# Performance work log

Measured on AMD Instinct MI355X. Metric: run time of the kernel, lower is better.

Reference implementation:

```python
import jax, jax.numpy as jnp
import numpy as np

V, H, F, E, S, N, O = 50000, 1024, 4096, 8, 128, 4096, 2


def setup_inputs() -> dict:
    key = jax.random.key(0)
    ks = jax.random.split(key, 9)
    x = jax.random.randint(ks[0], (N, S), 0, V)
    emb = jax.random.normal(ks[1], (V, H), dtype=jnp.float32) * 0.02
    emb = emb.at[0].set(0.0)  # padding_idx=0
    Wg = jax.random.normal(ks[2], (H, E), dtype=jnp.float32) * 0.02
    W1 = jax.random.normal(ks[3], (E, H, F), dtype=jnp.float32) * 0.02
    b1 = jnp.zeros((E, F), dtype=jnp.float32)
    W2 = jax.random.normal(ks[4], (E, F, H), dtype=jnp.float32) * 0.02
    b2 = jnp.zeros((E, H), dtype=jnp.float32)
    Wfc = jax.random.normal(ks[5], (H, O), dtype=jnp.float32) * 0.02
    bfc = jnp.zeros((O,), dtype=jnp.float32)
    return {"x": x, "emb": emb, "Wg": Wg, "W1": W1, "b1": b1,
            "W2": W2, "b2": b2, "Wfc": Wfc, "bfc": bfc}


def reference(x, emb, Wg, W1, b1, W2, b2, Wfc, bfc):
    # embedding lookup + mean pool over sequence: [N, S, H] -> [N, H]
    h = emb[x].mean(axis=1)
    # top-1 gating (deepspeed MoE default k=1)
    gates = jax.nn.softmax(h @ Wg, axis=-1)              # [N, E]
    idx = jnp.argmax(gates, axis=-1)                      # [N]
    onehot = jax.nn.one_hot(idx, E, dtype=h.dtype)        # [N, E]
    combine = gates * onehot                              # [N, E] top-1 prob
    # dense-dispatch reference for grouped expert GEMMs (FFN: H->F->H, ReLU)
    h1 = jax.nn.relu(jnp.einsum('nh,ehf->nef', h, W1) + b1)  # [N, E, F]
    h2 = jnp.einsum('nef,efh->neh', h1, W2) + b2             # [N, E, H]
    moe = jnp.einsum('ne,neh->nh', combine, h2)              # [N, H]
    return jax.nn.log_softmax(moe @ Wfc + bfc, axis=1)       # [N, O]
```

## Files before the change

kernel.cpp:

```cpp
#include <hip/hip_runtime.h>
#include <stdint.h>

#define V_SZ 50000
#define H_DIM 1024
#define F_DIM 4096
#define E_NUM 8
#define S_LEN 128
#define N_TOK 4096
#define NPAD (N_TOK + E_NUM*128)
#define EMB_SCALE 16.0f
#define SK2 4

typedef unsigned short u16;
typedef unsigned int u32;
typedef unsigned char u8;
typedef short bf16x8 __attribute__((ext_vector_type(8)));
typedef float f32x4 __attribute__((ext_vector_type(4)));
typedef float f32x2 __attribute__((ext_vector_type(2)));

__device__ __forceinline__ u16 f2bf(float f) {
  u32 u = __builtin_bit_cast(u32, f);
  u += 0x7fffu + ((u >> 16) & 1u);
  return (u16)(u >> 16);
}
__device__ __forceinline__ u32 pack2(float a, float b) {
  return (u32)f2bf(a) | ((u32)f2bf(b) << 16);
}

__device__ __forceinline__ void gld_lds16(u16* lds, const u16* g) {
  __builtin_amdgcn_global_load_lds((const __attribute__((address_space(1))) void*)g,
                                   (__attribute__((address_space(3))) void*)lds,
                                   16, 0, 0);
}

__global__ void embconv_kernel(const float* __restrict__ emb, u8* __restrict__ embf8) {
  const size_t total = (size_t)V_SZ*H_DIM/8;
  const size_t stride = (size_t)gridDim.x*blockDim.x;
  for (size_t i = (size_t)blockIdx.x*blockDim.x + threadIdx.x; i < total; i += stride) {
    const float4 a = ((const float4*)emb)[i*2];
    const float4 b = ((const float4*)emb)[i*2+1];
    u32 w0, w1;
    w0 = __builtin_amdgcn_cvt_pk_fp8_f32(a.x*EMB_SCALE, a.y*EMB_SCALE, 0u, false);
    w0 = __builtin_amdgcn_cvt_pk_fp8_f32(a.z*EMB_SCALE, a.w*EMB_SCALE, w0, true);
    w1 = __builtin_amdgcn_cvt_pk_fp8_f32(b.x*EMB_SCALE, b.y*EMB_SCALE, 0u, false);
    w1 = __builtin_amdgcn_cvt_pk_fp8_f32(b.z*EMB_SCALE, b.w*EMB_SCALE, w1, true);
    ((uint2*)embf8)[i] = make_uint2(w0, w1);
  }
}

__global__ void poolgate_kernel(const int* __restrict__ x, const u8* __restrict__ embf8,
                                const float* __restrict__ Wg,
                                u16* __restrict__ hB, float* __restrict__ gate_val,
                                int* __restrict__ gate_idx, int* __restrict__ cnt) {
  __shared__ int sidx[S_LEN];
  __shared__ float wsum[4][8];
  const int n = blockIdx.x, t = threadIdx.x;
  if (t < S_LEN) sidx[t] = x[n*S_LEN + t];
  __syncthreads();
  float a0 = 0.f, a1 = 0.f, a2 = 0.f, a3 = 0.f;
  #pragma unroll 8
  for (int s = 0; s < S_LEN; ++s) {
    const u32 w = *(const u32*)(embf8 + (size_t)sidx[s]*H_DIM + t*4);
    const f32x2 lo = __builtin_amdgcn_cvt_pk_f32_fp8(w, false);
    const f32x2 hi = __builtin_amdgcn_cvt_pk_f32_fp8(w, true);
    a0 += lo[0]; a1 += lo[1]; a2 += hi[0]; a3 += hi[1];
  }
  const float sc = 1.0f/((float)S_LEN * EMB_SCALE);
  a0 *= sc; a1 *= sc; a2 *= sc; a3 *= sc;
  uint2 pk; pk.x = pack2(a0, a1); pk.y = pack2(a2, a3);
  *(uint2*)&hB[(size_t)n*H_DIM + t*4] = pk;
  float lg[E_NUM];
  #pragma unroll
  for (int e = 0; e < E_NUM; ++e) lg[e] = 0.f;
  const float hv[4] = {a0, a1, a2, a3};
  #pragma unroll
  for (int j = 0; j < 4; ++j) {
    const float4* w4 = (const float4*)(Wg + (size_t)(t*4+j)*E_NUM);
    const float4 wa = w4[0], wb = w4[1];
    lg[0] += hv[j]*wa.x; lg[1] += hv[j]*wa.y; lg[2] += hv[j]*wa.z; lg[3] += hv[j]*wa.w;
    lg[4] += hv[j]*wb.x; lg[5] += hv[j]*wb.y; lg[6] += hv[j]*wb.z; lg[7] += hv[j]*wb.w;
  }
  #pragma unroll
  for (int m = 32; m >= 1; m >>= 1) {
    #pragma unroll
    for (int e = 0; e < E_NUM; ++e) lg[e] += __shfl_xor(lg[e], m);
  }
  if ((t & 63) == 0) {
    #pragma unroll
    for (int e = 0; e < E_NUM; ++e) wsum[t >> 6][e] = lg[e];
  }
  __syncthreads();
  if (t == 0) {
    float l[E_NUM];
    #pragma unroll
    for (int e = 0; e < E_NUM; ++e)
      l[e] = wsum[0][e] + wsum[1][e] + wsum[2][e] + wsum[3][e];
    float mx = l[0]; int im = 0;
    #pragma unroll
    for (int e = 1; e < E_NUM; ++e) if (l[e] > mx) { mx = l[e]; im = e; }
    float s = 0.f;
    #pragma unroll
    for (int e = 0; e < E_NUM; ++e) s += expf(l[e] - mx);
    gate_val[n] = 1.0f / s;
    gate_idx[n] = im;
    atomicAdd(&cnt[im], 1);
  }
}

__global__ void offsets_kernel(const int* __restrict__ cnt, int* __restrict__ pad_off) {
  int o = 0;
  for (int e = 0; e < E_NUM; ++e) {
    pad_off[e] = o;
    o += ((cnt[e] + 127) >> 7) << 7;
  }
  pad_off[E_NUM] = o;
}

__global__ void scatterconv_kernel(const u16* __restrict__ hB, const int* __restrict__ gate_idx,
                                   const int* __restrict__ pad_off, int* __restrict__ cursor,
                                   int* __restrict__ perm, u16* __restrict__ Hg) {
  __shared__ int srow;
  const int n = blockIdx.x, t = threadIdx.x;
  if (t == 0) {
    const int e = gate_idx[n];
    const int pos = atomicAdd(&cursor[e], 1);
    const int row = pad_off[e] + pos;
    perm[row] = n;
    srow = row;
  }
  __syncthreads();
  const int row = srow;
  const uint4 v = *(const uint4*)(hB + (size_t)n*H_DIM + t*8);
  *(uint4*)&Hg[(size_t)row*H_DIM + t*8] = v;
}

template<int C, int RPER>
__global__ void ct_kernel(const float* __restrict__ in, u16* __restrict__ out) {
  __shared__ float tile[64][65];
  const int c0 = blockIdx.x*64, r0 = blockIdx.y*64;
  const int t = threadIdx.x;
  const int cq = t & 15, rr = t >> 4;
  #pragma unroll
  for (int p = 0; p < 4; ++p) {
    const int row = p*16 + rr;
    float4 v = ((const float4*)(in + (size_t)(r0+row)*C + c0))[cq];
    tile[row][cq*4+0] = v.x; tile[row][cq*4+1] = v.y;
    tile[row][cq*4+2] = v.z; tile[row][cq*4+3] = v.w;
  }
  __syncthreads();
  const int slot = t & 7, nn = t >> 3;
  const int e = r0 / RPER, rl0 = r0 % RPER;
  u16* outE = out + (size_t)e*C*RPER;
  #pragma unroll
  for (int p = 0; p < 2; ++p) {
    const int nc = p*32 + nn;
    uint4 q;
    q.x = pack2(tile[slot*8+0][nc], tile[slot*8+1][nc]);
    q.y = pack2(tile[slot*8+2][nc], tile[slot*8+3][nc]);
    q.z = pack2(tile[slot*8+4][nc], tile[slot*8+5][nc]);
    q.w = pack2(tile[slot*8+6][nc], tile[slot*8+7][nc]);
    *(uint4*)&outE[(size_t)(c0+nc)*RPER + rl0 + slot*8] = q;
  }
}

template<int KTOT, int EPI, int SK>
__launch_bounds__(256, 2)
__global__ void gemm_kernel(const u16* __restrict__ A, const u16* __restrict__ B,
                            const float* __restrict__ bias,
                            const int* __restrict__ perm,
                            const int* __restrict__ pad_off,
                            const int* __restrict__ cnt,
                            u16* __restrict__ out_bf, float* __restrict__ out_f) {
  constexpr int MD = (EPI == 1) ? F_DIM : H_DIM;
  const int e  = blockIdx.z / SK;
  const int kc = blockIdx.z % SK;
  const int seg0 = pad_off[e], seg1 = pad_off[e+1];
  if ((int)blockIdx.y*128 >= seg1 - seg0) return;
  const int t0 = seg0 + blockIdx.y*128;
  const int f0 = blockIdx.x*128;
  const u16* Ae = A + (size_t)e*MD*KTOT;

  __shared__ u16 As[128*64];
  __shared__ u16 Bs[128*64];

  const int tid = threadIdx.x;
  const int lane = tid & 63, wave = tid >> 6;
  const int wm = wave >> 1, wn = wave & 1;

  f32x4 acc[4][4];
  #pragma unroll
  for (int i = 0; i < 4; ++i)
    #pragma unroll
    for (int j = 0; j < 4; ++j) acc[i][j] = (f32x4){0.f, 0.f, 0.f, 0.f};

  const int rsub = lane >> 3, slot = lane & 7;
  const int csw = slot ^ rsub;
  const int fr = lane & 15, fg = lane >> 4;

  const int kbeg = kc*(KTOT/SK), kend = kbeg + KTOT/SK;
  for (int kk = kbeg; kk < kend; kk += 64) {
    __syncthreads();
    #pragma unroll
    for (int i = 0; i < 4; ++i) {
      const int chunk = wave*4 + i;
      const int r = chunk*8 + rsub;
      gld_lds16(&As[chunk*512], Ae + (size_t)(f0 + r)*KTOT + kk + csw*8);
      gld_lds16(&Bs[chunk*512], B  + (size_t)(t0 + r)*KTOT + kk + csw*8);
    }
    __syncthreads();
    #pragma unroll
    for (int kh = 0; kh < 2; ++kh) {
      bf16x8 av[4], bv[4];
      #pragma unroll
      for (int mi = 0; mi < 4; ++mi) {
        const int ra = wm*64 + mi*16 + fr;
        const int sa = (kh*4 + fg) ^ (ra & 7);
        av[mi] = *(const bf16x8*)&As[ra*64 + sa*8];
      }
      #pragma unroll
      for (int ni = 0; ni < 4; ++ni) {
        const int rb = wn*64 + ni*16 + fr;
        const int sb = (kh*4 + fg) ^ (rb & 7);
        bv[ni] = *(const bf16x8*)&Bs[rb*64 + sb*8];
      }
      #pragma unroll
      for (int mi = 0; mi < 4; ++mi)
        #pragma unroll
        for (int ni = 0; ni < 4; ++ni)
          acc[mi][ni] = __builtin_amdgcn_mfma_f32_16x16x32_bf16(av[mi], bv[ni], acc[mi][ni], 0, 0, 0);
    }
  }

  #pragma unroll
  for (int mi = 0; mi < 4; ++mi) {
    const int gm0 = f0 + wm*64 + mi*16 + fg*4;
    #pragma unroll
    for (int ni = 0; ni < 4; ++ni) {
      const int gn = wn*64 + ni*16 + fr;
      if constexpr (EPI == 1) {
        const float* bp = bias + (size_t)e*MD + gm0;
        const float v0 = fmaxf(acc[mi][ni][0] + bp[0], 0.f);
        const float v1 = fmaxf(acc[mi][ni][1] + bp[1], 0.f);
        const float v2 = fmaxf(acc[mi][ni][2] + bp[2], 0.f);
        const float v3 = fmaxf(acc[mi][ni][3] + bp[3], 0.f);
        uint2 pk; pk.x = pack2(v0, v1); pk.y = pack2(v2, v3);
        *(uint2*)&out_bf[(size_t)(t0 + gn)*F_DIM + gm0] = pk;
      } else {
        const int local = blockIdx.y*128 + gn;
        if (local < cnt[e]) {
          const int tok = perm[t0 + gn];
          float* plane = out_f + (size_t)kc*N_TOK*H_DIM;
          *(f32x4*)&plane[(size_t)tok*H_DIM + gm0] = acc[mi][ni];
        }
      }
    }
  }
}

__global__ void final_kernel(const float* __restrict__ planes,
                             const float* __restrict__ b2,
                             const int* __restrict__ gate_idx,
                             const float* __restrict__ gate_val,
                             const float* __restrict__ Wfc,
                             const float* __restrict__ bfc, float* __restrict__ out) {
  const int n = blockIdx.x, l = threadIdx.x;
  const int e = gate_idx[n];
  const float g = gate_val[n];
  const size_t pstride = (size_t)N_TOK*H_DIM/4;
  const float4* p0 = (const float4*)planes + (size_t)n*(H_DIM/4);
  const float4* b24 = (const float4*)(b2 + (size_t)e*H_DIM);
  const float2* w2 = (const float2*)Wfc;
  float a0 = 0.f, a1 = 0.f;
  #pragma unroll
  for (int j = 0; j < H_DIM/256; ++j) {
    const int i4 = j*64 + l;
    const float4 q0 = p0[i4];
    const float4 q1 = p0[i4 + pstride];
    const float4 q2 = p0[i4 + 2*pstride];
    const float4 q3 = p0[i4 + 3*pstride];
    const float4 bb = b24[i4];
    const float vx = (q0.x+q1.x+q2.x+q3.x + bb.x)*g;
    const float vy = (q0.y+q1.y+q2.y+q3.y + bb.y)*g;
    const float vz = (q0.z+q1.z+q2.z+q3.z + bb.z)*g;
    const float vw = (q0.w+q1.w+q2.w+q3.w + bb.w)*g;
    const int hh = i4*4;
    const float2 r0 = w2[hh], r1 = w2[hh+1], r2 = w2[hh+2], r3 = w2[hh+3];
    a0 += vx*r0.x + vy*r1.x + vz*r2.x + vw*r3.x;
    a1 += vx*r0.y + vy*r1.y + vz*r2.y + vw*r3.y;
  }
  #pragma unroll
  for (int m = 32; m >= 1; m >>= 1) { a0 += __shfl_xor(a0, m); a1 += __shfl_xor(a1, m); }
  if (l == 0) {
    const float l0 = a0 + bfc[0], l1 = a1 + bfc[1];
    const float mx = fmaxf(l0, l1);
    const float lse = mx + logf(expf(l0 - mx) + expf(l1 - mx));
    out[(size_t)n*2 + 0] = l0 - lse;
    out[(size_t)n*2 + 1] = l1 - lse;
  }
}

extern "C" void kernel_launch(void* const* d_in, const int* in_sizes, int n_in,
                              void* d_out, int out_size, void* d_ws, size_t ws_size,
                              hipStream_t stream) {
  const int*   x   = (const int*)  d_in[0];
  const float* emb = (const float*)d_in[1];
  const float* Wg  = (const float*)d_in[2];
  const float* W1  = (const float*)d_in[3];
  const float* b1  = (const float*)d_in[4];
  const float* W2  = (const float*)d_in[5];
  const float* b2  = (const float*)d_in[6];
  const float* Wfc = (const float*)d_in[7];
  const float* bfc = (const float*)d_in[8];
  float* out = (float*)d_out;

  char* p = (char*)d_ws;
  size_t off = 0;
  auto alloc = [&](size_t bytes) {
    void* r = p + off;
    off = (off + bytes + 255) & ~(size_t)255;
    return r;
  };
  u16*   hB       = (u16*)  alloc((size_t)N_TOK*H_DIM*2);
  float* gate_val = (float*)alloc((size_t)N_TOK*4);
  int*   gate_idx = (int*)  alloc((size_t)N_TOK*4);
  int*   perm     = (int*)  alloc((size_t)NPAD*4);
  int*   meta     = (int*)  alloc(256);
  int* cnt = meta; int* cursor = meta + 8; int* pad_off = meta + 16;
  u16* Hg  = (u16*)alloc((size_t)NPAD*H_DIM*2);
  u16* H1  = (u16*)alloc((size_t)NPAD*F_DIM*2);
  char* uni = (char*)alloc((size_t)E_NUM*F_DIM*H_DIM*2*2);
  u8*  embf8  = (u8*)uni;
  u16* W1T    = (u16*)uni;
  u16* W2T    = W1T + (size_t)E_NUM*F_DIM*H_DIM;
  float* planes = (float*)uni;

  hipMemsetAsync(meta, 0, 256, stream);
  embconv_kernel<<<4096, 256, 0, stream>>>(emb, embf8);
  poolgate_kernel<<<N_TOK, 256, 0, stream>>>(x, embf8, Wg, hB, gate_val, gate_idx, cnt);
  offsets_kernel<<<1, 1, 0, stream>>>(cnt, pad_off);
  scatterconv_kernel<<<N_TOK, 128, 0, stream>>>(hB, gate_idx, pad_off, cursor, perm, Hg);
  ct_kernel<F_DIM, H_DIM><<<dim3(F_DIM/64, E_NUM*H_DIM/64), 256, 0, stream>>>(W1, W1T);
  ct_kernel<H_DIM, F_DIM><<<dim3(H_DIM/64, E_NUM*F_DIM/64), 256, 0, stream>>>(W2, W2T);
  gemm_kernel<H_DIM, 1, 1><<<dim3(F_DIM/128, 32, E_NUM), 256, 0, stream>>>(
      W1T, Hg, b1, nullptr, pad_off, cnt, H1, nullptr);
  gemm_kernel<F_DIM, 2, SK2><<<dim3(H_DIM/128, 32, E_NUM*SK2), 256, 0, stream>>>(
      W2T, H1, nullptr, perm, pad_off, cnt, nullptr, planes);
  final_kernel<<<N_TOK, 64, 0, stream>>>(planes, b2, gate_idx, gate_val, Wfc, bfc, out);
}
```

Measured before the change: 756.6 us.

## Fuse Wfc projection into second expert GEMM epilogue with atomic logit accumulation

The second expert GEMM no longer writes four split-K fp32 planes of shape N×H. Instead its epilogue projects each accumulator tile onto the two-column Wfc, scales by the gate value, and atomically adds into a per-token logits buffer. The b2 contribution is precomputed per expert as a dot with Wfc and seeded into the logits during the scatter kernel. A tiny log-softmax kernel replaces the plane-reading final kernel. This removes roughly 64MB of plane writes and reads, at the cost of many float atomics and nondeterministic summation order.

New measurement: 764.2 us. No clear change (+1.0%).

```diff
diff --git a/kernel.cpp b/kernel.cpp
--- a/kernel.cpp
+++ b/kernel.cpp
@@ -116,9 +116,27 @@
   pad_off[E_NUM] = o;
 }
 
+__global__ void biasdot_kernel(const float* __restrict__ b2, const float* __restrict__ Wfc,
+                               float* __restrict__ bdot) {
+  const int e = blockIdx.x, l = threadIdx.x;
+  float s0 = 0.f, s1 = 0.f;
+  for (int h = l; h < H_DIM; h += 64) {
+    const float v = b2[(size_t)e*H_DIM + h];
+    const float2 w = ((const float2*)Wfc)[h];
+    s0 += v*w.x; s1 += v*w.y;
+  }
+  #pragma unroll
+  for (int m = 32; m >= 1; m >>= 1) { s0 += __shfl_xor(s0, m); s1 += __shfl_xor(s1, m); }
+  if (l == 0) { bdot[e*2] = s0; bdot[e*2+1] = s1; }
+}
+
 __global__ void scatterconv_kernel(const u16* __restrict__ hB, const int* __restrict__ gate_idx,
                                    const int* __restrict__ pad_off, int* __restrict__ cursor,
-                                   int* __restrict__ perm, u16* __restrict__ Hg) {
+                                   int* __restrict__ perm, u16* __restrict__ Hg,
+                                   const float* __restrict__ gate_val,
+                                   const float* __restrict__ bdot,
+                                   const float* __restrict__ bfc,
+                                   float* __restrict__ logits) {
   __shared__ int srow;
   const int n = blockIdx.x, t = threadIdx.x;
   if (t == 0) {
@@ -128,6 +146,10 @@
     perm[row] = n;
     srow = row;
   }
+  if (t < 2) {
+    const int e = gate_idx[n];
+    logits[(size_t)n*2 + t] = bfc[t] + gate_val[n]*bdot[e*2 + t];
+  }
   __syncthreads();
   const int row = srow;
   const uint4 v = *(const uint4*)(hB + (size_t)n*H_DIM + t*8);
@@ -170,7 +192,10 @@
                             const int* __restrict__ perm,
                             const int* __restrict__ pad_off,
                             const int* __restrict__ cnt,
-                            u16* __restrict__ out_bf, float* __restrict__ out_f) {
+                            u16* __restrict__ out_bf,
+                            const float* __restrict__ gate_val,
+                            const float* __restrict__ Wfc,
+                            float* __restrict__ logits) {
   constexpr int MD = (EPI == 1) ? F_DIM : H_DIM;
   const int e  = blockIdx.z / SK;
   const int kc = blockIdx.z % SK;
@@ -231,72 +256,59 @@
     }
   }
 
-  #pragma unroll
-  for (int mi = 0; mi < 4; ++mi) {
-    const int gm0 = f0 + wm*64 + mi*16 + fg*4;
-    #pragma unroll
-    for (int ni = 0; ni < 4; ++ni) {
-      const int gn = wn*64 + ni*16 + fr;
-      if constexpr (EPI == 1) {
-        const float* bp = bias + (size_t)e*MD + gm0;
+  if constexpr (EPI == 1) {
+    #pragma unroll
+    for (int mi = 0; mi < 4; ++mi) {
+      const int gm0 = f0 + wm*64 + mi*16 + fg*4;
+      const float* bp = bias + (size_t)e*MD + gm0;
+      #pragma unroll
+      for (int ni = 0; ni < 4; ++ni) {
+        const int gn = wn*64 + ni*16 + fr;
         const float v0 = fmaxf(acc[mi][ni][0] + bp[0], 0.f);
         const float v1 = fmaxf(acc[mi][ni][1] + bp[1], 0.f);
         const float v2 = fmaxf(acc[mi][ni][2] + bp[2], 0.f);
         const float v3 = fmaxf(acc[mi][ni][3] + bp[3], 0.f);
         uint2 pk; pk.x = pack2(v0, v1); pk.y = pack2(v2, v3);
         *(uint2*)&out_bf[(size_t)(t0 + gn)*F_DIM + gm0] = pk;
-      } else {
-        const int local = blockIdx.y*128 + gn;
-        if (local < cnt[e]) {
-          const int tok = perm[t0 + gn];
-          float* plane = out_f + (size_t)kc*N_TOK*H_DIM;
-          *(f32x4*)&plane[(size_t)tok*H_DIM + gm0] = acc[mi][ni];
+      }
+    }
+  } else {
+    const float2* wfc2 = (const float2*)Wfc;
+    #pragma unroll
+    for (int ni = 0; ni < 4; ++ni) {
+      float p0 = 0.f, p1 = 0.f;
+      #pragma unroll
+      for (int mi = 0; mi < 4; ++mi) {
+        const int gm0 = f0 + wm*64 + mi*16 + fg*4;
+        #pragma unroll
+        for (int j = 0; j < 4; ++j) {
+          const float2 wv = wfc2[gm0 + j];
+          p0 += acc[mi][ni][j]*wv.x;
+          p1 += acc[mi][ni][j]*wv.y;
         }
       }
+      p0 += __shfl_xor(p0, 16); p0 += __shfl_xor(p0, 32);
+      p1 += __shfl_xor(p1, 16); p1 += __shfl_xor(p1, 32);
+      const int gn = wn*64 + ni*16 + fr;
+      const int local = blockIdx.y*128 + gn;
+      if (fg == 0 && local < cnt[e]) {
+        const int tok = perm[t0 + gn];
+        const float g = gate_val[tok];
+        atomicAdd(&logits[(size_t)tok*2 + 0], p0*g);
+        atomicAdd(&logits[(size_t)tok*2 + 1], p1*g);
+      }
     }
   }
 }
 
-__global__ void final_kernel(const float* __restrict__ planes,
-                             const float* __restrict__ b2,
-                             const int* __restrict__ gate_idx,
-                             const float* __restrict__ gate_val,
-                             const float* __restrict__ Wfc,
-                             const float* __restrict__ bfc, float* __restrict__ out) {
-  const int n = blockIdx.x, l = threadIdx.x;
-  const int e = gate_idx[n];
-  const float g = gate_val[n];
-  const size_t pstride = (size_t)N_TOK*H_DIM/4;
-  const float4* p0 = (const float4*)planes + (size_t)n*(H_DIM/4);
-  const float4* b24 = (const float4*)(b2 + (size_t)e*H_DIM);
-  const float2* w2 = (const float2*)Wfc;
-  float a0 = 0.f, a1 = 0.f;
-  #pragma unroll
-  for (int j = 0; j < H_DIM/256; ++j) {
-    const int i4 = j*64 + l;
-    const float4 q0 = p0[i4];
-    const float4 q1 = p0[i4 + pstride];
-    const float4 q2 = p0[i4 + 2*pstride];
-    const float4 q3 = p0[i4 + 3*pstride];
-    const float4 bb = b24[i4];
-    const float vx = (q0.x+q1.x+q2.x+q3.x + bb.x)*g;
-    const float vy = (q0.y+q1.y+q2.y+q3.y + bb.y)*g;
-    const float vz = (q0.z+q1.z+q2.z+q3.z + bb.z)*g;
-    const float vw = (q0.w+q1.w+q2.w+q3.w + bb.w)*g;
-    const int hh = i4*4;
-    const float2 r0 = w2[hh], r1 = w2[hh+1], r2 = w2[hh+2], r3 = w2[hh+3];
-    a0 += vx*r0.x + vy*r1.x + vz*r2.x + vw*r3.x;
-    a1 += vx*r0.y + vy*r1.y + vz*r2.y + vw*r3.y;
-  }
-  #pragma unroll
-  for (int m = 32; m >= 1; m >>= 1) { a0 += __shfl_xor(a0, m); a1 += __shfl_xor(a1, m); }
-  if (l == 0) {
-    const float l0 = a0 + bfc[0], l1 = a1 + bfc[1];
-    const float mx = fmaxf(l0, l1);
-    const float lse = mx + logf(expf(l0 - mx) + expf(l1 - mx));
-    out[(size_t)n*2 + 0] = l0 - lse;
-    out[(size_t)n*2 + 1] = l1 - lse;
-  }
+__global__ void lsm_kernel(const float* __restrict__ logits, float* __restrict__ out) {
+  const int n = blockIdx.x*blockDim.x + threadIdx.x;
+  if (n >= N_TOK) return;
+  const float l0 = logits[(size_t)n*2], l1 = logits[(size_t)n*2 + 1];
+  const float mx = fmaxf(l0, l1);
+  const float lse = mx + logf(expf(l0 - mx) + expf(l1 - mx));
+  out[(size_t)n*2 + 0] = l0 - lse;
+  out[(size_t)n*2 + 1] = l1 - lse;
 }
 
 extern "C" void kernel_launch(void* const* d_in, const int* in_sizes, int n_in,
@@ -324,6 +336,8 @@
   float* gate_val = (float*)alloc((size_t)N_TOK*4);
   int*   gate_idx = (int*)  alloc((size_t)N_TOK*4);
   int*   perm     = (int*)  alloc((size_t)NPAD*4);
+  float* logits   = (float*)alloc((size_t)N_TOK*2*4);
+  float* bdot     = (float*)alloc(256);
   int*   meta     = (int*)  alloc(256);
   int* cnt = meta; int* cursor = meta + 8; int* pad_off = meta + 16;
   u16* Hg  = (u16*)alloc((size_t)NPAD*H_DIM*2);
@@ -332,18 +346,19 @@
   u8*  embf8  = (u8*)uni;
   u16* W1T    = (u16*)uni;
   u16* W2T    = W1T + (size_t)E_NUM*F_DIM*H_DIM;
-  float* planes = (float*)uni;
 
   hipMemsetAsync(meta, 0, 256, stream);
   embconv_kernel<<<4096, 256, 0, stream>>>(emb, embf8);
   poolgate_kernel<<<N_TOK, 256, 0, stream>>>(x, embf8, Wg, hB, gate_val, gate_idx, cnt);
   offsets_kernel<<<1, 1, 0, stream>>>(cnt, pad_off);
-  scatterconv_kernel<<<N_TOK, 128, 0, stream>>>(hB, gate_idx, pad_off, cursor, perm, Hg);
+  biasdot_kernel<<<E_NUM, 64, 0, stream>>>(b2, Wfc, bdot);
+  scatterconv_kernel<<<N_TOK, 128, 0, stream>>>(hB, gate_idx, pad_off, cursor, perm, Hg,
+                                                gate_val, bdot, bfc, logits);
   ct_kernel<F_DIM, H_DIM><<<dim3(F_DIM/64, E_NUM*H_DIM/64), 256, 0, stream>>>(W1, W1T);
   ct_kernel<H_DIM, F_DIM><<<dim3(H_DIM/64, E_NUM*F_DIM/64), 256, 0, stream>>>(W2, W2T);
   gemm_kernel<H_DIM, 1, 1><<<dim3(F_DIM/128, 32, E_NUM), 256, 0, stream>>>(
-      W1T, Hg, b1, nullptr, pad_off, cnt, H1, nullptr);
+      W1T, Hg, b1, nullptr, pad_off, cnt, H1, nullptr, nullptr, nullptr);
   gemm_kernel<F_DIM, 2, SK2><<<dim3(H_DIM/128, 32, E_NUM*SK2), 256, 0, stream>>>(
-      W2T, H1, nullptr, perm, pad_off, cnt, nullptr, planes);
-  final_kernel<<<N_TOK, 64, 0, stream>>>(planes, b2, gate_idx, gate_val, Wfc, bfc, out);
-}
+      W2T, H1, nullptr, perm, pad_off, cnt, nullptr, gate_val, Wfc, logits);
+  lsm_kernel<<<(N_TOK + 255)/256, 256, 0, stream>>>(logits, out);
+}
```
